# Optimization experiments

Hardware: AMD Instinct MI355X
Metric: run time of the kernel (lower is better)

Reference implementation:

```python
import jax, jax.numpy as jnp
import numpy as np

B, S, D = 4, 2048, 512

def setup_inputs() -> dict:
    key = jax.random.key(0)
    ks = jax.random.split(key, 7)
    # scale weights so unscaled logits stay in a sane softmax range
    w_scale = 0.05
    return {
        "x": jax.random.normal(ks[0], (B, S, D), dtype=jnp.float32),
        "W_q": jax.random.normal(ks[1], (D, D), dtype=jnp.float32) * w_scale,
        "W_k": jax.random.normal(ks[2], (D, D), dtype=jnp.float32) * w_scale,
        "W_v": jax.random.normal(ks[3], (D, D), dtype=jnp.float32) * w_scale,
        "b_q": jax.random.normal(ks[4], (D,), dtype=jnp.float32) * w_scale,
        "b_k": jax.random.normal(ks[5], (D,), dtype=jnp.float32) * w_scale,
        "b_v": jax.random.normal(ks[6], (D,), dtype=jnp.float32) * w_scale,
    }

def reference(x, W_q, W_k, W_v, b_q, b_k, b_v):
    # QKV projections: [B,S,D] @ [D,D] + [D]
    q = jnp.einsum('bsd,de->bse', x, W_q) + b_q
    k = jnp.einsum('bsd,de->bse', x, W_k) + b_k
    v = jnp.einsum('bsd,de->bse', x, W_v) + b_v
    # unscaled attention scores [B,S,S]
    scores = jnp.einsum('bqd,bkd->bqk', q, k)
    attn = jax.nn.softmax(scores, axis=-1)
    # weighted sum of values [B,S,D]
    return jnp.einsum('bqk,bkd->bqd', attn, v)
```

## Files before the change

### kernel.cpp

```cpp
#include <hip/hip_runtime.h>
#include <hip/hip_bf16.h>
#include <hip/hip_fp16.h>

#define BB 4
#define SS 2048
#define DD 512

typedef short s16x8 __attribute__((ext_vector_type(8)));
typedef short s16x4 __attribute__((ext_vector_type(4)));
typedef float f32x4 __attribute__((ext_vector_type(4)));
typedef _Float16 f16x8 __attribute__((ext_vector_type(8)));

__device__ __forceinline__ short f2h(float f) {
    const _Float16 h = (_Float16)f;
    union { _Float16 h; short s; } u; u.h = h; return u.s;
}
__device__ __forceinline__ float h2f(short s) {
    union { short s; _Float16 h; } u; u.s = s; return (float)u.h;
}
__device__ __forceinline__ f16x8 as_h(s16x8 v) {
    union { s16x8 s; f16x8 h; } u; u.s = v; return u.h;
}

__device__ __forceinline__ void gload_lds16(const void* g, void* l) {
    __builtin_amdgcn_global_load_lds(
        (const __attribute__((address_space(1))) void*)g,
        (__attribute__((address_space(3))) void*)l, 16, 0, 0);
}

__global__ __launch_bounds__(512, 2) void qkt256(
    const short* __restrict__ qf, const short* __restrict__ kf,
    short* __restrict__ outS, int nwg)
{
    __shared__ short lds[65536];

    const int tid = threadIdx.x;
    const int wave = tid >> 6, lane = tid & 63;
    const int flat = blockIdx.x + 8 * blockIdx.y + 64 * blockIdx.z;
    const int w = (flat & 7) * (nwg >> 3) + (flat >> 3);
    const int bm = ((w >> 3) & 7) * 256, bn = (w & 7) * 256;
    const long z = w >> 6;
    qf += z * (long)SS * DD; kf += z * (long)SS * DD;
    outS += z * (long)SS * SS;

    const int wm = (wave >> 2) * 128, wn = (wave & 3) * 64;
    const int lrow = lane & 15, lk16 = (lane >> 4) * 16;

    f32x4 acc[8][4] = {};

    auto base = [&](int buf, int arr) -> short* { return &lds[(buf * 2 + arr) * 8192]; };
    auto issue = [&](int buf, int arr, int k0) {
#pragma unroll
        for (int h = 0; h < 2; h++) {
            const int Lb = (h << 13) + (wave << 10) + (lane << 4);
            const int Ls = Lb ^ (((Lb >> 7) & 3) << 4);
            const int row = Ls >> 6, elem = (Ls & 63) >> 1;
            const short* s = arr ? kf : qf;
            const int rb = arr ? bn : bm;
            gload_lds16(s + (size_t)(rb + row) * DD + k0 + elem,
                        (char*)base(buf, arr) + Lb);
        }
    };
    auto rd = [&](int buf, int arr, int row) -> s16x8 {
        const int L = (row << 6) + lk16;
        const int Ls = L ^ (((L >> 7) & 3) << 4);
        return *(const s16x8*)((const char*)base(buf, arr) + Ls);
    };

#define QK_TILE(T, CUR, Bc, Bn, PREF)                                            \
  {                                                                              \
    _Pragma("unroll")                                                            \
    for (int p = 0; p < 4; p++) {                                                \
      const s16x8 ah0 = rd(CUR, 0, wm + (p * 2 + 0) * 16 + lrow);                \
      const s16x8 ah1 = rd(CUR, 0, wm + (p * 2 + 1) * 16 + lrow);                \
      if (PREF && p == 0) { issue((CUR) ^ 1, 1, ((T) + 1) * 32); }               \
      if (PREF && p == 1) { issue((CUR) ^ 1, 0, ((T) + 1) * 32); }               \
      if (PREF && p == 3) {                                                      \
        __builtin_amdgcn_sched_barrier(0);       \
        _Pragma("unroll")                                                        \
        for (int n = 0; n < 4; n++) {                                            \
          Bn[n] = rd((CUR) ^ 1, 1, wn + n * 16 + lrow);                          \
        }                                                                        \
      }                                                                          \
      __builtin_amdgcn_s_barrier();                                              \
      if (PREF && p == 3) { asm volatile("s_waitcnt lgkmcnt(4)" ::: "memory"); } \
      else                { asm volatile("s_waitcnt lgkmcnt(0)" ::: "memory"); } \
      __builtin_amdgcn_sched_barrier(0);                                         \
      __builtin_amdgcn_s_setprio(1);                                             \
      _Pragma("unroll")                                                          \
      for (int q = 0; q < 2; q++) {                                              \
        const s16x8 af = q ? ah1 : ah0;                                          \
        _Pragma("unroll")                                                        \
        for (int n = 0; n < 4; n++) {                                            \
          acc[p * 2 + q][n] = __builtin_amdgcn_mfma_f32_16x16x32_f16(            \
              as_h(af), as_h(Bc[n]), acc[p * 2 + q][n], 0, 0, 0);                \
        }                                                                        \
      }                                                                          \
      __builtin_amdgcn_s_setprio(0);                                             \
      if (PREF && p == 2) { asm volatile("s_waitcnt vmcnt(2)" ::: "memory");     \
                            __builtin_amdgcn_sched_barrier(0); }                 \
      if (PREF && p == 3) { asm volatile("s_waitcnt vmcnt(0)" ::: "memory");     \
                            __builtin_amdgcn_sched_barrier(0); }                 \
      __builtin_amdgcn_s_barrier();                                              \
    }                                                                            \
  }

    issue(0, 1, 0); issue(0, 0, 0);
    asm volatile("s_waitcnt vmcnt(0)" ::: "memory");
    __builtin_amdgcn_s_barrier();
    s16x8 bE[4], bO[4];
#pragma unroll
    for (int n = 0; n < 4; n++) bE[n] = rd(0, 1, wn + n * 16 + lrow);

    for (int t = 0; t < 14; t += 2) {
        QK_TILE(t,     0, bE, bO, 1);
        QK_TILE(t + 1, 1, bO, bE, 1);
    }
    QK_TILE(14, 0, bE, bO, 1);
    QK_TILE(15, 1, bO, bE, 0);
#undef QK_TILE

    __syncthreads();
    short* ebuf = &lds[0];
#pragma unroll
    for (int m = 0; m < 8; m++) {
#pragma unroll
        for (int n = 0; n < 4; n++) {
#pragma unroll
            for (int j = 0; j < 4; j++) {
                const int rl = wm + m * 16 + (lane >> 4) * 4 + j;
                const int cl = wn + n * 16 + lrow;
                const int pcb = (cl >> 3) ^ ((rl & 3) << 1);
                ebuf[rl * 256 + pcb * 8 + (cl & 7)] =
                    (short)__float2int_rn(acc[m][n][j] * 128.0f);
            }
        }
    }
    __syncthreads();
#pragma unroll
    for (int it = 0; it < 16; it++) {
        const int u = it * 512 + tid;
        const int R = u >> 5, cb = u & 31;
        const int pcb = cb ^ ((R & 3) << 1);
        const s16x8 val = *(const s16x8*)&ebuf[R * 256 + pcb * 8];
        *(s16x8*)&outS[(size_t)(bm + R) * SS + bn + cb * 8] = val;
    }
}

__global__ __launch_bounds__(256, 3) void proj_all(
    const short* __restrict__ xh, const short* __restrict__ xl,
    const short* __restrict__ wt,
    const float* __restrict__ bq, const float* __restrict__ bk,
    const float* __restrict__ bv,
    short* __restrict__ qfp, short* __restrict__ kfp, short* __restrict__ vt)
{
    __shared__ short As[2][128 * 64];
    __shared__ short Bs[128 * 64];

    const int tid = threadIdx.x;
    const int wave = tid >> 6, lane = tid & 63;
    const int wsel = blockIdx.x >> 2;
    const int bnl = (blockIdx.x & 3) * 128;
    const int bm = blockIdx.y * 128;
    const bool lo = (wsel < 2);
    const short* B0 = wt + (size_t)wsel * DD * DD;
    const float* bias = (wsel == 0) ? bq : (wsel == 1) ? bk : bv;

    f32x4 acc[4][4] = {};
    const int wm = (wave >> 1) * 64, wn = (wave & 1) * 64;
    const int lrow = lane & 15, lk = (lane >> 4) * 8;

    auto swz = [](int L) { return L ^ (((L >> 7) & 7) << 4); };

    for (int k0 = 0; k0 < DD; k0 += 64) {
        if (k0) __syncthreads();
#pragma unroll
        for (int r = 0; r < 4; r++) {
            const int L = tid * 16 + r * 4096;
            const int Ls = swz(L);
            const int row = Ls >> 7, col = (Ls & 127) >> 1;
            gload_lds16(xh + (size_t)(bm + row) * DD + k0 + col, (char*)&As[0][0] + L);
            gload_lds16(B0 + (size_t)(bnl + row) * DD + k0 + col, (char*)&Bs[0] + L);
            if (lo)
                gload_lds16(xl + (size_t)(bm + row) * DD + k0 + col, (char*)&As[1][0] + L);
        }
        __syncthreads();

#pragma unroll
        for (int kk = 0; kk < 64; kk += 32) {
            s16x8 ah[4], bh[4], al[4];
#pragma unroll
            for (int m = 0; m < 4; m++)
                ah[m] = *(const s16x8*)((const char*)&As[0][0] +
                        swz(((wm + m * 16 + lrow) * 64 + kk + lk) * 2));
#pragma unroll
            for (int n = 0; n < 4; n++)
                bh[n] = *(const s16x8*)((const char*)&Bs[0] +
                        swz(((wn + n * 16 + lrow) * 64 + kk + lk) * 2));
            if (lo) {
#pragma unroll
                for (int m = 0; m < 4; m++)
                    al[m] = *(const s16x8*)((const char*)&As[1][0] +
                            swz(((wm + m * 16 + lrow) * 64 + kk + lk) * 2));
            }
#pragma unroll
            for (int m = 0; m < 4; m++) {
#pragma unroll
                for (int n = 0; n < 4; n++) {
                    acc[m][n] = __builtin_amdgcn_mfma_f32_16x16x32_f16(
                        as_h(ah[m]), as_h(bh[n]), acc[m][n], 0, 0, 0);
                    if (lo)
                        acc[m][n] = __builtin_amdgcn_mfma_f32_16x16x32_f16(
                            as_h(al[m]), as_h(bh[n]), acc[m][n], 0, 0, 0);
                }
            }
        }
    }

    __syncthreads();
    short* cbuf = &As[0][0];
#pragma unroll
    for (int m = 0; m < 4; m++) {
#pragma unroll
        for (int n = 0; n < 4; n++) {
#pragma unroll
            for (int j = 0; j < 4; j++) {
                const int rl = wm + m * 16 + (lane >> 4) * 4 + j;
                const int cl = wn + n * 16 + lrow;
                const float v = acc[m][n][j] + bias[bnl + cl];
                if (wsel < 2)
                    cbuf[rl * 128 + (cl ^ ((rl & 7) << 3))] = f2h(v);
                else
                    cbuf[cl * 128 + (rl ^ ((cl & 7) << 3))] = f2h(v);
            }
        }
    }
    __syncthreads();
    if (wsel < 2) {
        short* outp = wsel ? kfp : qfp;
#pragma unroll
        for (int it = 0; it < 8; it++) {
            const int u = it * 256 + tid;
            const int r = u >> 4, c8 = (u & 15) * 8;
            const s16x8 val = *(const s16x8*)&cbuf[r * 128 + (c8 ^ ((r & 7) << 3))];
            *(s16x8*)&outp[(size_t)(bm + r) * DD + bnl + c8] = val;
        }
    } else {
        const int b = bm >> 11, s0 = bm & 2047;
#pragma unroll
        for (int it = 0; it < 8; it++) {
            const int idx = it * 256 + tid;
            const int dd = idx >> 4, c8 = (idx & 15) * 8;
            const s16x8 val = *(const s16x8*)&cbuf[dd * 128 + (c8 ^ ((dd & 7) << 3))];
            *(s16x8*)&vt[((size_t)b << 20) + ((size_t)(bnl + dd) << 11) + s0 + c8] = val;
        }
    }
}

__global__ __launch_bounds__(256, 2) void pv_gemm(
    const short* __restrict__ P, const short* __restrict__ vt,
    float* __restrict__ out)
{
    __shared__ short As[64 * 64];
    __shared__ short Bs[128 * 64];

    const int tid = threadIdx.x;
    const int wave = tid >> 6, lane = tid & 63;
    const int bm = blockIdx.y * 64, bn = blockIdx.x * 128;
    const long z = blockIdx.z;
    P += z * (long)SS * SS;
    vt += z << 20;
    out += z * (long)SS * DD;

    f32x4 acc[2][4] = {};
    const int wm = (wave >> 1) * 32, wn = (wave & 1) * 64;
    const int lrow = lane & 15, lk = (lane >> 4) * 8;

    auto swz = [](int L) { return L ^ (((L >> 7) & 7) << 4); };

    for (int k0 = 0; k0 < SS; k0 += 64) {
        if (k0) __syncthreads();
#pragma unroll
        for (int r = 0; r < 2; r++) {
            const int L = tid * 16 + r * 4096;
            const int Ls = swz(L);
            const int row = Ls >> 7, col = (Ls & 127) >> 1;
            gload_lds16(P + (size_t)(bm + row) * SS + k0 + col, (char*)&As[0] + L);
        }
#pragma unroll
        for (int r = 0; r < 4; r++) {
            const int L = tid * 16 + r * 4096;
            const int Ls = swz(L);
            const int row = Ls >> 7, col = (Ls & 127) >> 1;
            gload_lds16(vt + ((size_t)(bn + row) << 11) + k0 + col, (char*)&Bs[0] + L);
        }
        __syncthreads();

#pragma unroll
        for (int kk = 0; kk < 64; kk += 32) {
            s16x8 a[2], b[4];
#pragma unroll
            for (int m = 0; m < 2; m++)
                a[m] = *(const s16x8*)((const char*)&As[0] +
                       swz(((wm + m * 16 + lrow) * 64 + kk + lk) * 2));
#pragma unroll
            for (int n = 0; n < 4; n++)
                b[n] = *(const s16x8*)((const char*)&Bs[0] +
                       swz(((wn + n * 16 + lrow) * 64 + kk + lk) * 2));
#pragma unroll
            for (int m = 0; m < 2; m++)
#pragma unroll
                for (int n = 0; n < 4; n++)
                    acc[m][n] = __builtin_amdgcn_mfma_f32_16x16x32_f16(
                        as_h(a[m]), as_h(b[n]), acc[m][n], 0, 0, 0);
        }
    }

#pragma unroll
    for (int m = 0; m < 2; m++) {
#pragma unroll
        for (int n = 0; n < 4; n++) {
#pragma unroll
            for (int j = 0; j < 4; j++) {
                const int row = bm + wm + m * 16 + (lane >> 4) * 4 + j;
                const int col = bn + wn + n * 16 + lrow;
                out[(size_t)row * DD + col] = acc[m][n][j];
            }
        }
    }
}

__global__ __launch_bounds__(256) void cast_all(
    const float* __restrict__ x,
    const float* __restrict__ wq, const float* __restrict__ wk,
    const float* __restrict__ wv,
    short* __restrict__ xh, short* __restrict__ xl,
    short* __restrict__ wt)
{
    const int bid = blockIdx.x;
    if (bid < 4096) {
        const int i = bid * 256 + threadIdx.x;
        const float4 v = ((const float4*)x)[i];
        const float vv[4] = {v.x, v.y, v.z, v.w};
        s16x4 h, l;
#pragma unroll
        for (int j = 0; j < 4; j++) {
            const short hh = f2h(vv[j]);
            h[j] = hh;
            l[j] = f2h(vv[j] - h2f(hh));
        }
        ((s16x4*)xh)[i] = h;
        ((s16x4*)xl)[i] = l;
    } else {
        const int t = (bid - 4096) * 256 + threadIdx.x;
        const int w = t >> 18;
        const int r = t & 262143;
        const float* src = (w == 0) ? wq : ((w == 1) ? wk : wv);
        const float v = src[r];
        const int k = r >> 9, n = r & 511;
        wt[((size_t)w << 18) + ((size_t)n << 9) + k] = f2h(v);
    }
}

__global__ __launch_bounds__(256) void softmax_rows(
    const short* __restrict__ S, short* __restrict__ P)
{
    const int row = blockIdx.x;
    const long z = blockIdx.y;
    const short* s = S + z * (long)SS * SS + (long)row * SS;
    short* p = P + z * (long)SS * SS + (long)row * SS;
    const int tid = threadIdx.x;

    const s16x8 raw = ((const s16x8*)s)[tid];
    float v[8];
#pragma unroll
    for (int j = 0; j < 8; j++) v[j] = (float)(int)raw[j] * 0.0078125f;

    float m = v[0];
#pragma unroll
    for (int j = 1; j < 8; j++) m = fmaxf(m, v[j]);
#pragma unroll
    for (int off = 32; off >= 1; off >>= 1) m = fmaxf(m, __shfl_xor(m, off));
    __shared__ float redm[4], reds[4];
    if ((tid & 63) == 0) redm[tid >> 6] = m;
    __syncthreads();
    m = fmaxf(fmaxf(redm[0], redm[1]), fmaxf(redm[2], redm[3]));

    float e[8], sum = 0.f;
#pragma unroll
    for (int j = 0; j < 8; j++) { e[j] = __expf(v[j] - m); sum += e[j]; }
#pragma unroll
    for (int off = 32; off >= 1; off >>= 1) sum += __shfl_xor(sum, off);
    if ((tid & 63) == 0) reds[tid >> 6] = sum;
    __syncthreads();
    sum = reds[0] + reds[1] + reds[2] + reds[3];
    const float inv = 1.0f / sum;

    s16x8 o;
#pragma unroll
    for (int j = 0; j < 8; j++) o[j] = f2h(e[j] * inv);
    ((s16x8*)p)[tid] = o;
}

extern "C" void kernel_launch(void* const* d_in, const int* in_sizes, int n_in,
                              void* d_out, int out_size, void* d_ws, size_t ws_size,
                              hipStream_t stream)
{
    const float* x  = (const float*)d_in[0];
    const float* Wq = (const float*)d_in[1];
    const float* Wk = (const float*)d_in[2];
    const float* Wv = (const float*)d_in[3];
    const float* bq = (const float*)d_in[4];
    const float* bk = (const float*)d_in[5];
    const float* bv = (const float*)d_in[6];
    float* out = (float*)d_out;

    const size_t MK = (size_t)BB * SS * DD;
    char* ws = (char*)d_ws;
    short* xh  = (short*)ws; ws += MK * 2;
    short* xl  = (short*)ws; ws += MK * 2;
    short* wt  = (short*)ws; ws += 3ull * DD * DD * 2;
    short* qfp = (short*)ws; ws += MK * 2;
    short* kfp = (short*)ws; ws += MK * 2;
    short* vt  = (short*)ws; ws += MK * 2;
    const size_t fixed = (size_t)(ws - (char*)d_ws);

    int g = 4;
    while (g > 0 && fixed + (size_t)g * ((size_t)SS * SS * 2 + (size_t)SS * SS * 2) > ws_size)
        g >>= 1;
    if (g == 0) return;
    short* sc = (short*)ws;
    short* P  = (short*)(ws + (size_t)g * SS * SS * 2);

    cast_all<<<dim3(7168), 256, 0, stream>>>(x, Wq, Wk, Wv, xh, xl, wt);
    proj_all<<<dim3(12, 64), 256, 0, stream>>>(xh, xl, wt, bq, bk, bv,
                                               qfp, kfp, vt);

    for (int b0 = 0; b0 < BB; b0 += g) {
        const int gg = (b0 + g <= BB) ? g : (BB - b0);
        qkt256<<<dim3(8, 8, gg), 512, 0, stream>>>(
            qfp + (size_t)b0 * SS * DD, kfp + (size_t)b0 * SS * DD, sc, 64 * gg);
        softmax_rows<<<dim3(SS, gg), 256, 0, stream>>>(sc, P);
        pv_gemm<<<dim3(4, 32, gg), 256, 0, stream>>>(
            P, vt + ((size_t)b0 << 20), out + (size_t)b0 * SS * DD);
    }
}
```

Baseline: 116.6 us.

## Restructure QK tile loop into two half-phases with fewer barriers

```diff
diff --git a/kernel.cpp b/kernel.cpp
--- a/kernel.cpp
+++ b/kernel.cpp
@@ -69,40 +69,63 @@
 
 #define QK_TILE(T, CUR, Bc, Bn, PREF)                                            \
   {                                                                              \
-    _Pragma("unroll")                                                            \
-    for (int p = 0; p < 4; p++) {                                                \
-      const s16x8 ah0 = rd(CUR, 0, wm + (p * 2 + 0) * 16 + lrow);                \
-      const s16x8 ah1 = rd(CUR, 0, wm + (p * 2 + 1) * 16 + lrow);                \
-      if (PREF && p == 0) { issue((CUR) ^ 1, 1, ((T) + 1) * 32); }               \
-      if (PREF && p == 1) { issue((CUR) ^ 1, 0, ((T) + 1) * 32); }               \
-      if (PREF && p == 3) {                                                      \
-        __builtin_amdgcn_sched_barrier(0);       \
-        _Pragma("unroll")                                                        \
-        for (int n = 0; n < 4; n++) {                                            \
-          Bn[n] = rd((CUR) ^ 1, 1, wn + n * 16 + lrow);                          \
-        }                                                                        \
+                                            \
+    s16x8 aA0 = rd(CUR, 0, wm + 0 * 16 + lrow);                                  \
+    s16x8 aA1 = rd(CUR, 0, wm + 1 * 16 + lrow);                                  \
+    s16x8 aA2 = rd(CUR, 0, wm + 2 * 16 + lrow);                                  \
+    s16x8 aA3 = rd(CUR, 0, wm + 3 * 16 + lrow);                                  \
+    if (PREF) {                                                                  \
+      issue((CUR) ^ 1, 1, ((T) + 1) * 32);                          \
+      __builtin_amdgcn_sched_barrier(0);                                         \
+      issue((CUR) ^ 1, 0, ((T) + 1) * 32);                         \
+    }                                                                            \
+    __builtin_amdgcn_s_barrier();                                                \
+    asm volatile("s_waitcnt lgkmcnt(0)" ::: "memory");                           \
+    __builtin_amdgcn_sched_barrier(0);                                           \
+    __builtin_amdgcn_s_setprio(1);                                               \
+    {                                                                            \
+      _Pragma("unroll")                                                          \
+      for (int n = 0; n < 4; n++) {                                              \
+        acc[0][n] = __builtin_amdgcn_mfma_f32_16x16x32_f16(as_h(aA0), as_h(Bc[n]), acc[0][n], 0, 0, 0); \
+        acc[1][n] = __builtin_amdgcn_mfma_f32_16x16x32_f16(as_h(aA1), as_h(Bc[n]), acc[1][n], 0, 0, 0); \
+        acc[2][n] = __builtin_amdgcn_mfma_f32_16x16x32_f16(as_h(aA2), as_h(Bc[n]), acc[2][n], 0, 0, 0); \
+        acc[3][n] = __builtin_amdgcn_mfma_f32_16x16x32_f16(as_h(aA3), as_h(Bc[n]), acc[3][n], 0, 0, 0); \
       }                                                                          \
-      __builtin_amdgcn_s_barrier();                                              \
-      if (PREF && p == 3) { asm volatile("s_waitcnt lgkmcnt(4)" ::: "memory"); } \
-      else                { asm volatile("s_waitcnt lgkmcnt(0)" ::: "memory"); } \
-      __builtin_amdgcn_sched_barrier(0);                                         \
-      __builtin_amdgcn_s_setprio(1);                                             \
+    }                                                                            \
+    __builtin_amdgcn_s_setprio(0);                                               \
+    if (PREF) { asm volatile("s_waitcnt vmcnt(2)" ::: "memory");                 \
+                __builtin_amdgcn_sched_barrier(0); }                             \
+    __builtin_amdgcn_s_barrier();                                                \
+                                            \
+    aA0 = rd(CUR, 0, wm + 4 * 16 + lrow);                                        \
+    aA1 = rd(CUR, 0, wm + 5 * 16 + lrow);                                        \
+    aA2 = rd(CUR, 0, wm + 6 * 16 + lrow);                                        \
+    aA3 = rd(CUR, 0, wm + 7 * 16 + lrow);                                        \
+    if (PREF) {                                                                  \
+      __builtin_amdgcn_sched_barrier(0);    \
       _Pragma("unroll")                                                          \
-      for (int q = 0; q < 2; q++) {                                              \
-        const s16x8 af = q ? ah1 : ah0;                                          \
-        _Pragma("unroll")                                                        \
-        for (int n = 0; n < 4; n++) {                                            \
-          acc[p * 2 + q][n] = __builtin_amdgcn_mfma_f32_16x16x32_f16(            \
-              as_h(af), as_h(Bc[n]), acc[p * 2 + q][n], 0, 0, 0);                \
-        }                                                                        \
+      for (int n = 0; n < 4; n++) {                                              \
+        Bn[n] = rd((CUR) ^ 1, 1, wn + n * 16 + lrow);                            \
       }                                                                          \
-      __builtin_amdgcn_s_setprio(0);                                             \
-      if (PREF && p == 2) { asm volatile("s_waitcnt vmcnt(2)" ::: "memory");     \
-                            __builtin_amdgcn_sched_barrier(0); }                 \
-      if (PREF && p == 3) { asm volatile("s_waitcnt vmcnt(0)" ::: "memory");     \
-                            __builtin_amdgcn_sched_barrier(0); }                 \
-      __builtin_amdgcn_s_barrier();                                              \
     }                                                                            \
+    __builtin_amdgcn_s_barrier();                                                \
+    if (PREF) { asm volatile("s_waitcnt lgkmcnt(4)" ::: "memory"); }             \
+    else      { asm volatile("s_waitcnt lgkmcnt(0)" ::: "memory"); }             \
+    __builtin_amdgcn_sched_barrier(0);                                           \
+    __builtin_amdgcn_s_setprio(1);                                               \
+    {                                                                            \
+      _Pragma("unroll")                                                          \
+      for (int n = 0; n < 4; n++) {                                              \
+        acc[4][n] = __builtin_amdgcn_mfma_f32_16x16x32_f16(as_h(aA0), as_h(Bc[n]), acc[4][n], 0, 0, 0); \
+        acc[5][n] = __builtin_amdgcn_mfma_f32_16x16x32_f16(as_h(aA1), as_h(Bc[n]), acc[5][n], 0, 0, 0); \
+        acc[6][n] = __builtin_amdgcn_mfma_f32_16x16x32_f16(as_h(aA2), as_h(Bc[n]), acc[6][n], 0, 0, 0); \
+        acc[7][n] = __builtin_amdgcn_mfma_f32_16x16x32_f16(as_h(aA3), as_h(Bc[n]), acc[7][n], 0, 0, 0); \
+      }                                                                          \
+    }                                                                            \
+    __builtin_amdgcn_s_setprio(0);                                               \
+    if (PREF) { asm volatile("s_waitcnt vmcnt(0)" ::: "memory");                 \
+                __builtin_amdgcn_sched_barrier(0); }                             \
+    __builtin_amdgcn_s_barrier();                                                \
   }
 
     issue(0, 1, 0); issue(0, 0, 0);
```

Measured after the change: 118.1 us. About the same (+1.3%).
